# Performance work log

Hardware: AMD Instinct MI355X
Metric: run time of the kernel (lower is better)

The kernel has to match this reference:

```python
import jax, jax.numpy as jnp
import numpy as np

D_MODEL = 2048
N_HEADS = 16
D_KEY = D_MODEL // N_HEADS
ALIBI_SLOPE = 8.0
KEY_SCALE = D_KEY ** -0.5
B, S = 2, 2048


def setup_inputs() -> dict:
    key = jax.random.key(0)
    ks = jax.random.split(key, 12)
    sd = D_MODEL ** -0.5
    return {
        "states": jax.random.normal(ks[0], (B, S, D_MODEL), jnp.float32),
        "bias_mask": jax.random.normal(ks[1], (B, S, S), jnp.float32),
        # weights stored [in, out] (torch Linear applies x @ W.T + b)
        "wq": jax.random.normal(ks[2], (D_MODEL, D_MODEL), jnp.float32) * sd,
        "bq": jnp.zeros((D_MODEL,), jnp.float32),
        "wk": jax.random.normal(ks[3], (D_MODEL, D_MODEL), jnp.float32) * sd,
        "bk": jnp.zeros((D_MODEL,), jnp.float32),
        "wv": jax.random.normal(ks[4], (D_MODEL, D_MODEL), jnp.float32) * sd,
        "bv": jnp.zeros((D_MODEL,), jnp.float32),
        "wg": jax.random.normal(ks[5], (D_MODEL, N_HEADS), jnp.float32) * sd,
        "bg": jnp.zeros((N_HEADS,), jnp.float32),
        "wo": jax.random.normal(ks[6], (D_MODEL, D_MODEL), jnp.float32) * sd,
        "bo": jnp.zeros((D_MODEL,), jnp.float32),
    }


def reference(states, bias_mask, wq, bq, wk, bk, wv, bv, wg, bg, wo, bo):
    # head_scale = exp2(-(h+1)*alibi_slope/n_heads), non-trainable buffer
    head_scale = jnp.exp2(-(jnp.arange(N_HEADS, dtype=jnp.float32) + 1.0)
                          * ALIBI_SLOPE / N_HEADS)
    # [B, H, Q, K] bias with per-head ALiBi scaling
    bias = bias_mask[:, None, :, :] * head_scale[None, :, None, None]

    def heads(x, w, b):  # [B,S,D] -> [B,H,S,Dk]
        y = x @ w + b
        return y.reshape(x.shape[0], x.shape[1], N_HEADS, D_KEY).transpose(0, 2, 1, 3)

    q = heads(states, wq, bq)
    k = heads(states, wk, bk)
    v = heads(states, wv, bv)

    scores = jnp.einsum('bhqd,bhkd->bhqk', q, k) * KEY_SCALE + bias
    probs = jax.nn.softmax(scores, axis=-1)
    o = jnp.einsum('bhqk,bhkd->bqhd', probs, v)  # [B,S,H,Dk]

    g = jax.nn.sigmoid(states @ wg + bg)  # [B,S,H] head gate
    o = o * g[..., None]

    return o.reshape(o.shape[0], o.shape[1], D_MODEL) @ wo + bo
```

## Files before the change

### kernel.cpp

```cpp
#include <hip/hip_runtime.h>
#include <hip/hip_bf16.h>

#define SEQ 2048
#define DM 2048
#define NH 16
#define DK 128
#define LOG2E 1.4426950408889634f
#define QK_SCALE 0.08838834764831845f

typedef __attribute__((ext_vector_type(8))) short short8;
typedef __attribute__((ext_vector_type(4))) float f32x4;
typedef __attribute__((ext_vector_type(4))) unsigned short us4;

__device__ __forceinline__ unsigned short f2b(float f) {
  union { float f; unsigned u; } v; v.f = f;
  unsigned r = v.u + 0x7fffu + ((v.u >> 16) & 1u);
  return (unsigned short)(r >> 16);
}
__device__ __forceinline__ float b2f(unsigned short v) {
  union { unsigned u; float f; } x; x.u = ((unsigned)v) << 16; return x.f;
}

__device__ __forceinline__ void gl_lds16(const void* g, void* l) {
  __builtin_amdgcn_global_load_lds((const __attribute__((address_space(1))) void*)g,
                                   (__attribute__((address_space(3))) void*)l, 16, 0, 0);
}

#define SBAR()   __builtin_amdgcn_s_barrier()
#define SCHED0() __builtin_amdgcn_sched_barrier(0)
#define LGKM0()  asm volatile("s_waitcnt lgkmcnt(0)" ::: "memory")

__global__ __launch_bounds__(256) void cast2_bf16_kernel(const float* __restrict__ in0,
                                                         unsigned short* __restrict__ out0,
                                                         const float* __restrict__ in1,
                                                         unsigned short* __restrict__ out1) {
  int bid = blockIdx.x;
  const float* in = (bid < 4096) ? in0 : in1;
  unsigned short* out = (bid < 4096) ? out0 : out1;
  int i = ((bid < 4096) ? bid : bid - 4096) * 256 + threadIdx.x;
  const float4* p = (const float4*)in;
  float4 a = p[2*i], b = p[2*i+1];
  us4 r0, r1;
  r0[0]=f2b(a.x); r0[1]=f2b(a.y); r0[2]=f2b(a.z); r0[3]=f2b(a.w);
  r1[0]=f2b(b.x); r1[1]=f2b(b.y); r1[2]=f2b(b.z); r1[3]=f2b(b.w);
  us4* o = (us4*)out;
  o[2*i] = r0; o[2*i+1] = r1;
}

__global__ __launch_bounds__(256) void transpose_cast4_kernel(const float* __restrict__ w0,
                                                              const float* __restrict__ w1,
                                                              const float* __restrict__ w2,
                                                              const float* __restrict__ w3,
                                                              unsigned short* __restrict__ dst) {
  const float* w = (blockIdx.z == 0) ? w0 : (blockIdx.z == 1) ? w1 : (blockIdx.z == 2) ? w2 : w3;
  unsigned short* wt = dst + (size_t)blockIdx.z * DM * DM;
  __shared__ float t[64][65];
  int c0 = blockIdx.x * 64, r0 = blockIdx.y * 64;
  int tid = threadIdx.x;
  int rr = tid >> 4;
  int c4 = (tid & 15) * 4;
#pragma unroll
  for (int p = 0; p < 4; ++p) {
    int r = p*16 + rr;
    float4 v = *(const float4*)&w[(size_t)(r0 + r)*DM + c0 + c4];
    t[r][c4] = v.x; t[r][c4+1] = v.y; t[r][c4+2] = v.z; t[r][c4+3] = v.w;
  }
  __syncthreads();
#pragma unroll
  for (int p = 0; p < 4; ++p) {
    int c = p*16 + rr;
    us4 v;
    v[0] = f2b(t[c4+0][c]); v[1] = f2b(t[c4+1][c]);
    v[2] = f2b(t[c4+2][c]); v[3] = f2b(t[c4+3][c]);
    *(us4*)&wt[(size_t)(c0 + c)*DM + r0 + c4] = v;
  }
}

__global__ __launch_bounds__(256) void transpose_wg_kernel(const float* __restrict__ wg,
                                                           unsigned short* __restrict__ wgT) {
  int idx = blockIdx.x * 256 + threadIdx.x;
  int c = idx & 15;
  int r0 = (idx >> 4) * 4;
#pragma unroll
  for (int r = 0; r < 4; ++r)
    wgT[(size_t)c*DM + r0 + r] = f2b(wg[(size_t)(r0 + r)*NH + c]);
}

__device__ __forceinline__ void gemm128_core(const unsigned short* __restrict__ A,
                                             const unsigned short* __restrict__ Bt,
                                             int m0, int n0, f32x4 (&acc)[4][4]) {
  __shared__ __align__(16) unsigned short Ab[2][8192];
  __shared__ __align__(16) unsigned short Bb[2][2][8192];
  const int TK = DM / 64;

  int tid = threadIdx.x, wid = tid >> 6, lane = tid & 63;
  int lo = lane & 15, hi = lane >> 4;
  int wm = wid >> 2, wn = wid & 3;
  int w2 = wid * 2;

  int srow8 = lane >> 3;
  int skb = (((lane & 7) ^ srow8) << 4);
  const char* Ag = (const char*)A;
  const char* Bg = (const char*)Bt;

#define STG_A(S,CUR) do {                                                          \
    const char* g = Ag + (size_t)(S)*128 + skb;                                    \
    char* l = (char*)&Ab[CUR][0] + w2*1024;                                        \
    gl_lds16(g + (size_t)(m0 + w2*8 + srow8)*4096,     l);                         \
    gl_lds16(g + (size_t)(m0 + w2*8 + 8 + srow8)*4096, l + 1024);                  \
  } while(0)
#define STG_B(S,CUR) do {                                                          \
    const char* g = Bg + (size_t)(S)*128 + skb;                                    \
    char* l = (char*)&Bb[CUR][0][0] + w2*1024;                                     \
    gl_lds16(g + (size_t)(n0 + w2*8 + srow8)*4096,           l);                   \
    gl_lds16(g + (size_t)(n0 + w2*8 + 8 + srow8)*4096,       l + 1024);            \
    gl_lds16(g + (size_t)(n0 + 128 + w2*8 + srow8)*4096,     l + 16384);           \
    gl_lds16(g + (size_t)(n0 + 128 + w2*8 + 8 + srow8)*4096, l + 16384 + 1024);    \
  } while(0)

#pragma unroll
  for (int i = 0; i < 4; ++i)
#pragma unroll
    for (int j = 0; j < 4; ++j) acc[i][j] = (f32x4){0.f,0.f,0.f,0.f};

  STG_B(0,0); STG_A(0,0); STG_B(1,1); STG_A(1,1);
  asm volatile("s_waitcnt vmcnt(6)" ::: "memory");
  SBAR();

  int msk = (lo & 7) << 4;
  int k0 = (hi*16) ^ msk;
  int k1 = (64 + hi*16) ^ msk;
  int brow = (wn & 1) * 64;

  short8 a[4][2], bA[2][2], bB[2][2];

#define MF8(MH,NHH,BF)                                                              \
  __builtin_amdgcn_s_setprio(1);                                                    \
  _Pragma("unroll") for (int mm = 0; mm < 2; ++mm)                                  \
  _Pragma("unroll") for (int nn = 0; nn < 2; ++nn) {                                \
    acc[(MH)*2+mm][(NHH)*2+nn] = __builtin_amdgcn_mfma_f32_16x16x32_bf16(           \
        a[(MH)*2+mm][0], BF[nn][0], acc[(MH)*2+mm][(NHH)*2+nn], 0, 0, 0);           \
    acc[(MH)*2+mm][(NHH)*2+nn] = __builtin_amdgcn_mfma_f32_16x16x32_bf16(           \
        a[(MH)*2+mm][1], BF[nn][1], acc[(MH)*2+mm][(NHH)*2+nn], 0, 0, 0);           \
  }                                                                                 \
  __builtin_amdgcn_s_setprio(0);

  for (int s = 0; s < TK; ++s) {
    int cur = s & 1;
    const char* Ac = (const char*)&Ab[cur][0];
    const char* Bc = (const char*)&Bb[cur][wn >> 1][0];
    bool pre = (s + 2) < TK;

#pragma unroll
    for (int mm = 0; mm < 4; ++mm) {
      a[mm][0] = *(const short8*)(Ac + (wm*64 + mm*16 + lo)*128 + k0);
      a[mm][1] = *(const short8*)(Ac + (wm*64 + mm*16 + lo)*128 + k1);
    }
#pragma unroll
    for (int nn = 0; nn < 2; ++nn) {
      bA[nn][0] = *(const short8*)(Bc + (brow + nn*16 + lo)*128 + k0);
      bA[nn][1] = *(const short8*)(Bc + (brow + nn*16 + lo)*128 + k1);
    }
    SBAR(); LGKM0(); SCHED0();
    MF8(0, 0, bA);
    SBAR();

#pragma unroll
    for (int nn = 0; nn < 2; ++nn) {
      bB[nn][0] = *(const short8*)(Bc + (brow + (2+nn)*16 + lo)*128 + k0);
      bB[nn][1] = *(const short8*)(Bc + (brow + (2+nn)*16 + lo)*128 + k1);
    }
    SBAR(); LGKM0(); SCHED0();
    MF8(0, 1, bB);
    SBAR();

    if (pre) STG_B(s + 2, cur);
    SBAR();
    MF8(1, 0, bA);
    SBAR();

    if (pre) {
      STG_A(s + 2, cur);
      asm volatile("s_waitcnt vmcnt(6)" ::: "memory");
    } else if (s == TK - 2) {
      asm volatile("s_waitcnt vmcnt(0)" ::: "memory");
    }
    SBAR();
    MF8(1, 1, bB);
    SBAR();
  }
#undef STG_A
#undef STG_B
#undef MF8
}

__global__ __launch_bounds__(512, 2) void gemm128_qkv_kernel(const unsigned short* __restrict__ A,
                                                             const unsigned short* __restrict__ Bt,
                                                             const float* __restrict__ bq,
                                                             const float* __restrict__ bk,
                                                             const float* __restrict__ bv,
                                                             unsigned short* __restrict__ QB,
                                                             unsigned short* __restrict__ KB,
                                                             unsigned short* __restrict__ VTB) {
  f32x4 acc[4][4];
  int n0 = blockIdx.x * 256, m0 = blockIdx.y * 128;
  gemm128_core(A, Bt, m0, n0, acc);

  int tid = threadIdx.x, wid = tid >> 6, lane = tid & 63;
  int lo = lane & 15, hi = lane >> 4;
  int wm = wid >> 2, wn = wid & 3;
  int m_base = m0 + wm*64;
  int n_base = n0 + wn*64;
  int sect = n0 >> 11;

  if (sect == 2) {
#pragma unroll
    for (int mi = 0; mi < 4; ++mi) {
      int m = m_base + mi*16 + 4*hi;
      int b = m >> 11, srow = m & 2047;
#pragma unroll
      for (int nf = 0; nf < 4; ++nf) {
        int n = n_base + nf*16 + lo;
        int nl = n & 2047, h = nl >> 7, d = nl & 127;
        float bvv = bv[nl];
        us4 pk;
#pragma unroll
        for (int r = 0; r < 4; ++r) pk[r] = f2b(acc[mi][nf][r] + bvv);
        *(us4*)&VTB[(((size_t)(b*NH + h))*DK + d)*SEQ + srow] = pk;
      }
    }
  } else {
    unsigned short* out = sect ? KB : QB;
    const float* bp = sect ? bk : bq;
    const float qs = sect ? 1.f : QK_SCALE * LOG2E;
#pragma unroll
    for (int mi = 0; mi < 4; ++mi) {
#pragma unroll
      for (int nf = 0; nf < 4; ++nf) {
        int n = n_base + nf*16 + lo;
        int nl = n & 2047, h = nl >> 7, d = nl & 127;
        float bvv = bp[nl];
#pragma unroll
        for (int r = 0; r < 4; ++r) {
          int m = m_base + mi*16 + 4*hi + r;
          int b = m >> 11, srow = m & 2047;
          out[(((size_t)(b*NH + h))*SEQ + srow)*DK + d] = f2b((acc[mi][nf][r] + bvv) * qs);
        }
      }
    }
  }
}

__global__ __launch_bounds__(512, 2) void gemm128_ao_kernel(const unsigned short* __restrict__ A,
                                                            const unsigned short* __restrict__ Bt,
                                                            const float* __restrict__ bias,
                                                            float* __restrict__ out) {
  f32x4 acc[4][4];
  int n0 = blockIdx.x * 256, m0 = blockIdx.y * 128;
  gemm128_core(A, Bt, m0, n0, acc);

  int tid = threadIdx.x, wid = tid >> 6, lane = tid & 63;
  int lo = lane & 15, hi = lane >> 4;
  int wm = wid >> 2, wn = wid & 3;
#pragma unroll
  for (int mi = 0; mi < 4; ++mi) {
#pragma unroll
    for (int nf = 0; nf < 4; ++nf) {
      int n = n0 + wn*64 + nf*16 + lo;
      float bvv = bias[n];
#pragma unroll
      for (int r = 0; r < 4; ++r) {
        int m = m0 + wm*64 + mi*16 + 4*hi + r;
        out[(size_t)m*DM + n] = acc[mi][nf][r] + bvv;
      }
    }
  }
}

__global__ __launch_bounds__(256) void gate_mfma_kernel(const unsigned short* __restrict__ XB,
                                                        const unsigned short* __restrict__ wgT,
                                                        const float* __restrict__ bg,
                                                        float* __restrict__ G) {
  int tid = threadIdx.x, wid = tid >> 6, lane = tid & 63;
  int lo = lane & 15, hi = lane >> 4;
  int m0 = blockIdx.x * 64 + wid * 16;

  f32x4 acc = {0.f, 0.f, 0.f, 0.f};
  const unsigned short* xrow = XB + (size_t)(m0 + lo) * DM + hi * 8;
  const unsigned short* grow = wgT + (size_t)lo * DM + hi * 8;
#pragma unroll 4
  for (int kt = 0; kt < DM; kt += 32) {
    short8 a = *(const short8*)(xrow + kt);
    short8 b = *(const short8*)(grow + kt);
    acc = __builtin_amdgcn_mfma_f32_16x16x32_bf16(a, b, acc, 0, 0, 0);
  }
  float bgv = bg[lo];
#pragma unroll
  for (int r = 0; r < 4; ++r) {
    float x = acc[r] + bgv;
    G[(size_t)(m0 + 4*hi + r) * NH + lo] = 1.f / (1.f + __builtin_amdgcn_exp2f(-x * LOG2E));
  }
}

__global__ __attribute__((amdgpu_flat_work_group_size(512,512)))
__attribute__((amdgpu_waves_per_eu(2,4)))
void attn_kernel(const unsigned short* __restrict__ Q,
                 const unsigned short* __restrict__ Kb,
                 const unsigned short* __restrict__ VT,
                 const unsigned short* __restrict__ biasb,
                 const float* __restrict__ G,
                 unsigned short* __restrict__ OG) {
  __shared__ __align__(16) unsigned short kbuf[2][64*128];
  __shared__ __align__(16) unsigned short vbuf[2][128*64];
  __shared__ __align__(16) unsigned short pbuf[8*16*64];

  int bid = blockIdx.x;
  int h  = bid & 15;
  int b  = (bid >> 4) & 1;
  int qt = bid >> 5;
  int bh = b*NH + h;

  int tid = threadIdx.x, wid = tid >> 6, lane = tid & 63;
  int lo = lane & 15, hi = lane >> 4;
  int qw0 = qt*128 + wid*16;

  float hs2 = __builtin_amdgcn_exp2f(-(float)(h+1) * 0.5f) * LOG2E;

  short8 qf[4];
#pragma unroll
  for (int ks = 0; ks < 4; ++ks)
    qf[ks] = *(const short8*)&Q[((size_t)bh*SEQ + qw0 + lo)*DK + ks*32 + hi*8];

  f32x4 zero4 = {0.f,0.f,0.f,0.f};
  f32x4 acco[8];
#pragma unroll
  for (int f = 0; f < 8; ++f) acco[f] = zero4;
  float lrun[4];
#pragma unroll
  for (int r = 0; r < 4; ++r) lrun[r] = 0.f;

  const char* kbase = (const char*)Kb + ((size_t)bh*SEQ)*DK*2;
  const char* vbase = (const char*)VT + ((size_t)bh*DK)*SEQ*2;
  const unsigned short* bb = biasb + ((size_t)b*SEQ + qw0 + 4*hi)*SEQ + lo;
  char* pb = (char*)pbuf + wid*2048;

  int s16 = lane >> 4, srow8 = lane >> 3;
  int kof = (lane & 15) * 16, vof = (lane & 7) * 16;
  int w2 = wid * 2;

#define STAGE_KV(KT, BUF) do {                                                        \
    _Pragma("unroll")                                                                 \
    for (int c = 0; c < 2; ++c) {                                                     \
      int krc = (w2 + c)*4 + s16;                                                     \
      gl_lds16(kbase + (size_t)((KT) + krc)*256 + (kof ^ ((krc & 7) << 4)),           \
               (char*)kbuf[BUF] + (w2 + c)*1024);                                     \
      int vrc = (w2 + c)*8 + srow8;                                                   \
      gl_lds16(vbase + (size_t)vrc*4096 + (size_t)(KT)*2 + (vof ^ (srow8 << 4)),      \
               (char*)vbuf[BUF] + (w2 + c)*1024);                                     \
    }                                                                                 \
  } while(0)

  unsigned short br[4][4];
#pragma unroll
  for (int r = 0; r < 4; ++r)
#pragma unroll
    for (int nf = 0; nf < 4; ++nf)
      br[r][nf] = bb[(size_t)r*SEQ + nf*16];
  STAGE_KV(0, 0);
  STAGE_KV(64, 1);
  asm volatile("s_waitcnt vmcnt(4)" ::: "memory");
  SBAR();

  const int NT = SEQ / 64;
  int cur = 0;
  for (int t = 0; t < NT; ++t) {
    f32x4 sf[4];
    __builtin_amdgcn_s_setprio(1);
#pragma unroll
    for (int nf = 0; nf < 4; ++nf) {
      f32x4 a = zero4;
#pragma unroll
      for (int ks = 0; ks < 4; ++ks) {
        int krw = nf*16 + lo;
        int cb = (ks*32 + hi*8)*2;
        short8 kf = *(const short8*)((const char*)kbuf[cur] + krw*256 + (cb ^ ((krw & 7) << 4)));
        a = __builtin_amdgcn_mfma_f32_16x16x32_bf16(qf[ks], kf, a, 0, 0, 0);
      }
      sf[nf] = a;
    }
    __builtin_amdgcn_s_setprio(0);

#pragma unroll
    for (int r = 0; r < 4; ++r) {
      int prow = 4*hi + r;
#pragma unroll
      for (int nf = 0; nf < 4; ++nf) {
        float s = fmaf(b2f(br[r][nf]), hs2, sf[nf][r]);
        float p = __builtin_amdgcn_exp2f(s);
        lrun[r] += p;
        *(unsigned short*)(pb + prow*128 + ((((nf*16 + lo)*2)) ^ ((prow & 7) << 4))) = f2b(p);
      }
    }

    short8 pf[2];
#pragma unroll
    for (int ks = 0; ks < 2; ++ks)
      pf[ks] = *(const short8*)(pb + lo*128 + ((ks*64 + hi*16) ^ ((lo & 7) << 4)));
    __builtin_amdgcn_s_setprio(1);
#pragma unroll
    for (int f = 0; f < 8; ++f) {
#pragma unroll
      for (int ks = 0; ks < 2; ++ks) {
        int vrw = f*16 + lo;
        int cb = (ks*32 + hi*8)*2;
        short8 vf = *(const short8*)((const char*)vbuf[cur] + vrw*128 + (cb ^ ((vrw & 7) << 4)));
        acco[f] = __builtin_amdgcn_mfma_f32_16x16x32_bf16(pf[ks], vf, acco[f], 0, 0, 0);
      }
    }
    __builtin_amdgcn_s_setprio(0);

    LGKM0(); SBAR();

    bool more1 = (t + 1) < NT;
    bool more2 = (t + 2) < NT;
    if (more1) {
      int ktn = (t + 1) * 64;
#pragma unroll
      for (int r = 0; r < 4; ++r)
#pragma unroll
        for (int nf = 0; nf < 4; ++nf)
          br[r][nf] = bb[(size_t)r*SEQ + ktn + nf*16];
    }
    if (more2) {
      STAGE_KV((t + 2) * 64, cur);
      asm volatile("s_waitcnt vmcnt(20)" ::: "memory");
    } else if (more1) {
      asm volatile("s_waitcnt vmcnt(16)" ::: "memory");
    }
    SBAR();
    cur ^= 1;
  }
#undef STAGE_KV

#pragma unroll
  for (int r = 0; r < 4; ++r) {
    float l = lrun[r];
    l += __shfl_xor(l, 1); l += __shfl_xor(l, 2);
    l += __shfl_xor(l, 4); l += __shfl_xor(l, 8);
    lrun[r] = l;
  }

#pragma unroll
  for (int r = 0; r < 4; ++r) {
    int qrow = qw0 + 4*hi + r;
    float inv = 1.f / lrun[r];
    float g = G[((size_t)(b*SEQ + qrow))*NH + h];
    float sgl = inv * g;
#pragma unroll
    for (int f = 0; f < 8; ++f)
      OG[((size_t)(b*SEQ) + qrow)*DM + h*DK + f*16 + lo] = f2b(acco[f][r] * sgl);
  }
}

extern "C" void kernel_launch(void* const* d_in, const int* in_sizes, int n_in,
                              void* d_out, int out_size, void* d_ws, size_t ws_size,
                              hipStream_t stream) {
  const float* states    = (const float*)d_in[0];
  const float* bias_mask = (const float*)d_in[1];
  const float* wq = (const float*)d_in[2];
  const float* bq = (const float*)d_in[3];
  const float* wk = (const float*)d_in[4];
  const float* bk = (const float*)d_in[5];
  const float* wv = (const float*)d_in[6];
  const float* bv = (const float*)d_in[7];
  const float* wg = (const float*)d_in[8];
  const float* bg = (const float*)d_in[9];
  const float* wo = (const float*)d_in[10];
  const float* bo = (const float*)d_in[11];

  char* ws = (char*)d_ws;
  unsigned short* XB   = (unsigned short*)(ws + 0);
  unsigned short* OGB  = XB;
  unsigned short* WQVT = (unsigned short*)(ws + 16777216UL);
  unsigned short* WOT  = (unsigned short*)(ws + 41943040UL);
  unsigned short* QB   = (unsigned short*)(ws + 50331648UL);
  unsigned short* KB   = (unsigned short*)(ws + 67108864UL);
  unsigned short* VTB  = (unsigned short*)(ws + 83886080UL);
  unsigned short* BIASB= (unsigned short*)(ws + 100663296UL);
  float*          GB   = (float*)         (ws + 117440512UL);
  unsigned short* WGT  = (unsigned short*)(ws + 117702656UL);

  cast2_bf16_kernel<<<8192, 256, 0, stream>>>(states, XB, bias_mask, BIASB);
  transpose_cast4_kernel<<<dim3(32, 32, 4), 256, 0, stream>>>(wq, wk, wv, wo, WQVT);
  transpose_wg_kernel<<<32, 256, 0, stream>>>(wg, WGT);

  gemm128_qkv_kernel<<<dim3(24, 32), 512, 0, stream>>>(XB, WQVT, bq, bk, bv, QB, KB, VTB);

  gate_mfma_kernel<<<64, 256, 0, stream>>>(XB, WGT, bg, GB);

  attn_kernel<<<512, 512, 0, stream>>>(QB, KB, VTB, BIASB, GB, OGB);

  gemm128_ao_kernel<<<dim3(8, 32), 512, 0, stream>>>(OGB, WOT, bo, (float*)d_out);
}
```

Baseline: 356.5 us.

## Process two 16-row query fragments per wave to double K/V tile reuse

Each wave now handles 32 query rows (two 16-row fragments) instead of 16, so each block covers 256 queries and the grid halves to 256 blocks. Every K/V tile staged in LDS is reused for twice as many query rows, which halves global K/V traffic and the number of barriers per unit of work. The cost is twice the accumulator, Q-fragment and bias registers per wave, which can lower occupancy. With 256 blocks on a GPU with 256 CUs there is also less parallelism left to hide latency, and the vmcnt wait thresholds were raised to account for the extra bias loads.

```diff
diff --git a/kernel.cpp b/kernel.cpp
--- a/kernel.cpp
+++ b/kernel.cpp
@@ -322,22 +322,28 @@
 
   int tid = threadIdx.x, wid = tid >> 6, lane = tid & 63;
   int lo = lane & 15, hi = lane >> 4;
-  int qw0 = qt*128 + wid*16;
+  int qw0 = qt*256 + wid*32;
 
   float hs2 = __builtin_amdgcn_exp2f(-(float)(h+1) * 0.5f) * LOG2E;
 
-  short8 qf[4];
-#pragma unroll
-  for (int ks = 0; ks < 4; ++ks)
-    qf[ks] = *(const short8*)&Q[((size_t)bh*SEQ + qw0 + lo)*DK + ks*32 + hi*8];
+  short8 qf[2][4];
+#pragma unroll
+  for (int f2 = 0; f2 < 2; ++f2)
+#pragma unroll
+    for (int ks = 0; ks < 4; ++ks)
+      qf[f2][ks] = *(const short8*)&Q[((size_t)bh*SEQ + qw0 + f2*16 + lo)*DK + ks*32 + hi*8];
 
   f32x4 zero4 = {0.f,0.f,0.f,0.f};
-  f32x4 acco[8];
-#pragma unroll
-  for (int f = 0; f < 8; ++f) acco[f] = zero4;
-  float lrun[4];
-#pragma unroll
-  for (int r = 0; r < 4; ++r) lrun[r] = 0.f;
+  f32x4 acco[2][8];
+#pragma unroll
+  for (int f2 = 0; f2 < 2; ++f2)
+#pragma unroll
+    for (int f = 0; f < 8; ++f) acco[f2][f] = zero4;
+  float lrun[2][4];
+#pragma unroll
+  for (int f2 = 0; f2 < 2; ++f2)
+#pragma unroll
+    for (int r = 0; r < 4; ++r) lrun[f2][r] = 0.f;
 
   const char* kbase = (const char*)Kb + ((size_t)bh*SEQ)*DK*2;
   const char* vbase = (const char*)VT + ((size_t)bh*DK)*SEQ*2;
@@ -360,12 +366,14 @@
     }                                                                                 \
   } while(0)
 
-  unsigned short br[4][4];
-#pragma unroll
-  for (int r = 0; r < 4; ++r)
-#pragma unroll
-    for (int nf = 0; nf < 4; ++nf)
-      br[r][nf] = bb[(size_t)r*SEQ + nf*16];
+  unsigned short br[2][4][4];
+#pragma unroll
+  for (int f2 = 0; f2 < 2; ++f2)
+#pragma unroll
+    for (int r = 0; r < 4; ++r)
+#pragma unroll
+      for (int nf = 0; nf < 4; ++nf)
+        br[f2][r][nf] = bb[(size_t)(f2*16 + r)*SEQ + nf*16];
   STAGE_KV(0, 0);
   STAGE_KV(64, 1);
   asm volatile("s_waitcnt vmcnt(4)" ::: "memory");
@@ -374,50 +382,53 @@
   const int NT = SEQ / 64;
   int cur = 0;
   for (int t = 0; t < NT; ++t) {
-    f32x4 sf[4];
-    __builtin_amdgcn_s_setprio(1);
-#pragma unroll
-    for (int nf = 0; nf < 4; ++nf) {
-      f32x4 a = zero4;
-#pragma unroll
-      for (int ks = 0; ks < 4; ++ks) {
-        int krw = nf*16 + lo;
-        int cb = (ks*32 + hi*8)*2;
-        short8 kf = *(const short8*)((const char*)kbuf[cur] + krw*256 + (cb ^ ((krw & 7) << 4)));
-        a = __builtin_amdgcn_mfma_f32_16x16x32_bf16(qf[ks], kf, a, 0, 0, 0);
+#pragma unroll
+    for (int f2 = 0; f2 < 2; ++f2) {
+      f32x4 sf[4];
+      __builtin_amdgcn_s_setprio(1);
+#pragma unroll
+      for (int nf = 0; nf < 4; ++nf) {
+        f32x4 a = zero4;
+#pragma unroll
+        for (int ks = 0; ks < 4; ++ks) {
+          int krw = nf*16 + lo;
+          int cb = (ks*32 + hi*8)*2;
+          short8 kf = *(const short8*)((const char*)kbuf[cur] + krw*256 + (cb ^ ((krw & 7) << 4)));
+          a = __builtin_amdgcn_mfma_f32_16x16x32_bf16(qf[f2][ks], kf, a, 0, 0, 0);
+        }
+        sf[nf] = a;
       }
-      sf[nf] = a;
-    }
-    __builtin_amdgcn_s_setprio(0);
-
-#pragma unroll
-    for (int r = 0; r < 4; ++r) {
-      int prow = 4*hi + r;
-#pragma unroll
-      for (int nf = 0; nf < 4; ++nf) {
-        float s = fmaf(b2f(br[r][nf]), hs2, sf[nf][r]);
-        float p = __builtin_amdgcn_exp2f(s);
-        lrun[r] += p;
-        *(unsigned short*)(pb + prow*128 + ((((nf*16 + lo)*2)) ^ ((prow & 7) << 4))) = f2b(p);
+      __builtin_amdgcn_s_setprio(0);
+
+#pragma unroll
+      for (int r = 0; r < 4; ++r) {
+        int prow = 4*hi + r;
+#pragma unroll
+        for (int nf = 0; nf < 4; ++nf) {
+          float s = fmaf(b2f(br[f2][r][nf]), hs2, sf[nf][r]);
+          float p = __builtin_amdgcn_exp2f(s);
+          lrun[f2][r] += p;
+          *(unsigned short*)(pb + prow*128 + ((((nf*16 + lo)*2)) ^ ((prow & 7) << 4))) = f2b(p);
+        }
       }
-    }
-
-    short8 pf[2];
-#pragma unroll
-    for (int ks = 0; ks < 2; ++ks)
-      pf[ks] = *(const short8*)(pb + lo*128 + ((ks*64 + hi*16) ^ ((lo & 7) << 4)));
-    __builtin_amdgcn_s_setprio(1);
-#pragma unroll
-    for (int f = 0; f < 8; ++f) {
-#pragma unroll
-      for (int ks = 0; ks < 2; ++ks) {
-        int vrw = f*16 + lo;
-        int cb = (ks*32 + hi*8)*2;
-        short8 vf = *(const short8*)((const char*)vbuf[cur] + vrw*128 + (cb ^ ((vrw & 7) << 4)));
-        acco[f] = __builtin_amdgcn_mfma_f32_16x16x32_bf16(pf[ks], vf, acco[f], 0, 0, 0);
+
+      short8 pf[2];
+#pragma unroll
+      for (int ks = 0; ks < 2; ++ks)
+        pf[ks] = *(const short8*)(pb + lo*128 + ((ks*64 + hi*16) ^ ((lo & 7) << 4)));
+      __builtin_amdgcn_s_setprio(1);
+#pragma unroll
+      for (int f = 0; f < 8; ++f) {
+#pragma unroll
+        for (int ks = 0; ks < 2; ++ks) {
+          int vrw = f*16 + lo;
+          int cb = (ks*32 + hi*8)*2;
+          short8 vf = *(const short8*)((const char*)vbuf[cur] + vrw*128 + (cb ^ ((vrw & 7) << 4)));
+          acco[f2][f] = __builtin_amdgcn_mfma_f32_16x16x32_bf16(pf[ks], vf, acco[f2][f], 0, 0, 0);
+        }
       }
-    }
-    __builtin_amdgcn_s_setprio(0);
+      __builtin_amdgcn_s_setprio(0);
+    }
 
     LGKM0(); SBAR();
 
@@ -426,16 +437,18 @@
     if (more1) {
       int ktn = (t + 1) * 64;
 #pragma unroll
-      for (int r = 0; r < 4; ++r)
-#pragma unroll
-        for (int nf = 0; nf < 4; ++nf)
-          br[r][nf] = bb[(size_t)r*SEQ + ktn + nf*16];
+      for (int f2 = 0; f2 < 2; ++f2)
+#pragma unroll
+        for (int r = 0; r < 4; ++r)
+#pragma unroll
+          for (int nf = 0; nf < 4; ++nf)
+            br[f2][r][nf] = bb[(size_t)(f2*16 + r)*SEQ + ktn + nf*16];
     }
     if (more2) {
       STAGE_KV((t + 2) * 64, cur);
-      asm volatile("s_waitcnt vmcnt(20)" ::: "memory");
+      asm volatile("s_waitcnt vmcnt(36)" ::: "memory");
     } else if (more1) {
-      asm volatile("s_waitcnt vmcnt(16)" ::: "memory");
+      asm volatile("s_waitcnt vmcnt(32)" ::: "memory");
     }
     SBAR();
     cur ^= 1;
@@ -443,23 +456,27 @@
 #undef STAGE_KV
 
 #pragma unroll
-  for (int r = 0; r < 4; ++r) {
-    float l = lrun[r];
-    l += __shfl_xor(l, 1); l += __shfl_xor(l, 2);
-    l += __shfl_xor(l, 4); l += __shfl_xor(l, 8);
-    lrun[r] = l;
-  }
-
-#pragma unroll
-  for (int r = 0; r < 4; ++r) {
-    int qrow = qw0 + 4*hi + r;
-    float inv = 1.f / lrun[r];
-    float g = G[((size_t)(b*SEQ + qrow))*NH + h];
-    float sgl = inv * g;
-#pragma unroll
-    for (int f = 0; f < 8; ++f)
-      OG[((size_t)(b*SEQ) + qrow)*DM + h*DK + f*16 + lo] = f2b(acco[f][r] * sgl);
-  }
+  for (int f2 = 0; f2 < 2; ++f2)
+#pragma unroll
+    for (int r = 0; r < 4; ++r) {
+      float l = lrun[f2][r];
+      l += __shfl_xor(l, 1); l += __shfl_xor(l, 2);
+      l += __shfl_xor(l, 4); l += __shfl_xor(l, 8);
+      lrun[f2][r] = l;
+    }
+
+#pragma unroll
+  for (int f2 = 0; f2 < 2; ++f2)
+#pragma unroll
+    for (int r = 0; r < 4; ++r) {
+      int qrow = qw0 + f2*16 + 4*hi + r;
+      float inv = 1.f / lrun[f2][r];
+      float g = G[((size_t)(b*SEQ + qrow))*NH + h];
+      float sgl = inv * g;
+#pragma unroll
+      for (int f = 0; f < 8; ++f)
+        OG[((size_t)(b*SEQ) + qrow)*DM + h*DK + f*16 + lo] = f2b(acco[f2][f][r] * sgl);
+    }
 }
 
 extern "C" void kernel_launch(void* const* d_in, const int* in_sizes, int n_in,
@@ -498,7 +515,7 @@
 
   gate_mfma_kernel<<<64, 256, 0, stream>>>(XB, WGT, bg, GB);
 
-  attn_kernel<<<512, 512, 0, stream>>>(QB, KB, VTB, BIASB, GB, OGB);
+  attn_kernel<<<256, 512, 0, stream>>>(QB, KB, VTB, BIASB, GB, OGB);
 
   gemm128_ao_kernel<<<dim3(8, 32), 512, 0, stream>>>(OGB, WOT, bo, (float*)d_out);
 }
```

Measured after the change: 338.9 us. 1.05x faster.
